# Optimization experiments

Measured on AMD Instinct MI355X. Metric: run time of the kernel, lower is better.

Reference implementation:

```python
import jax, jax.numpy as jnp
import numpy as np

N_SRC = 100000
N_DST = 100000
N_EDGES = 300000
FEAT = 256
REV_DIM = 128
REV_VOCAB = 500000


def setup_inputs() -> dict:
    key = jax.random.key(0)
    ks = jax.random.split(key, 14)
    feat = jax.random.normal(ks[0], (N_SRC, FEAT), dtype=jnp.float32)
    cj = jax.random.uniform(ks[1], (N_SRC, 1), dtype=jnp.float32)
    ci = jax.random.uniform(ks[2], (N_DST, 1), dtype=jnp.float32)
    edge_src = jax.random.randint(ks[3], (N_EDGES,), 0, N_SRC)
    edge_dst = jax.random.randint(ks[4], (N_EDGES,), 0, N_DST)
    review_id = jax.random.randint(ks[5], (N_EDGES,), 0, REV_VOCAB)
    s = 0.05
    review_emb = jax.random.normal(ks[6], (REV_VOCAB, REV_DIM), dtype=jnp.float32) * s
    prob_w = jax.random.normal(ks[7], (1, REV_DIM), dtype=jnp.float32) * s      # prob_score
    score_w = jax.random.normal(ks[8], (1, REV_DIM), dtype=jnp.float32) * s     # review_score
    rw1 = jax.random.normal(ks[9], (FEAT, REV_DIM), dtype=jnp.float32) * s      # review_w[0]
    rw2 = jax.random.normal(ks[10], (FEAT, FEAT), dtype=jnp.float32) * s        # review_w[2]
    rw3 = jax.random.normal(ks[11], (FEAT, FEAT), dtype=jnp.float32) * s        # review_w[4]
    lin_w = jax.random.normal(ks[12], (FEAT, FEAT), dtype=jnp.float32) * s      # self.linear
    lin_b = jax.random.normal(ks[13], (FEAT,), dtype=jnp.float32) * s
    return dict(feat=feat, cj=cj, ci=ci, edge_src=edge_src, edge_dst=edge_dst,
                review_id=review_id, review_emb=review_emb, prob_w=prob_w,
                score_w=score_w, rw1=rw1, rw2=rw2, rw3=rw3, lin_w=lin_w, lin_b=lin_b)


def reference(feat, cj, ci, edge_src, edge_dst, review_id,
              review_emb, prob_w, score_w, rw1, rw2, rw3, lin_w, lin_b):
    gelu = lambda x: jax.nn.gelu(x, approximate=False)  # torch default GELU (erf)
    # gather review embeddings per edge: [E, 128]
    rfeat = review_emb[review_id]
    pa = jax.nn.sigmoid(rfeat @ prob_w.T)    # [E, 1]
    ra = jax.nn.sigmoid(rfeat @ score_w.T)   # [E, 1]
    # review_w MLP: 128 -> F -> F -> F, no bias, GELU between
    rf = gelu(gelu(rfeat @ rw1.T) @ rw2.T) @ rw3.T  # [E, F]
    # per-edge message, gated and normalized by src cj (dropout is identity at p=0)
    m = (feat[edge_src] * pa + rf * ra) * cj[edge_src]  # [E, F]
    # scatter-sum to destination nodes
    h = jax.ops.segment_sum(m, edge_dst, num_segments=N_DST)  # [N_dst, F]
    rst = h * ci
    return rst @ lin_w.T + lin_b
```

## Files before the change

### kernel.cpp

```cpp
#include <hip/hip_runtime.h>
#include <math.h>
#include <stdint.h>


typedef short bf16x8 __attribute__((ext_vector_type(8)));
typedef float f32x16 __attribute__((ext_vector_type(16)));

__device__ __forceinline__ float bf2f(unsigned short v) {
    union { unsigned int u; float f; } x; x.u = ((unsigned int)v) << 16; return x.f;
}
__device__ __forceinline__ unsigned short f2bf(float f) {
    union { float f; unsigned int u; } x; x.f = f;
    unsigned int u = x.u;
    return (unsigned short)((u + 0x7FFFu + ((u >> 16) & 1u)) >> 16);
}
__device__ __forceinline__ unsigned pack2(float lo, float hi) {
    unsigned r;
    asm("v_cvt_pk_bf16_f32 %0, %1, %2" : "=v"(r) : "v"(lo), "v"(hi));
    return r;
}
__device__ __forceinline__ float gelu_fast(float x) {
    float e = __builtin_amdgcn_exp2f(x * -2.4554912f);
    return x * __builtin_amdgcn_rcpf(e + 1.0f);
}
__device__ __forceinline__ float sigmoidf(float x) {
    return 1.0f / (1.0f + expf(-x));
}

__global__ __launch_bounds__(256) void prep_weights(
    const float* __restrict__ rw1, const float* __restrict__ rw2,
    const float* __restrict__ rw3, const float* __restrict__ lw,
    unsigned short* __restrict__ w1s, unsigned short* __restrict__ w2s,
    unsigned short* __restrict__ w3s, unsigned short* __restrict__ lws)
{
    int i = blockIdx.x * blockDim.x + threadIdx.x;
    int j   = i & 7;
    int l   = (i >> 3) & 31;
    int kgg = (i >> 8) & 1;
    int n2  = (i >> 9) & 7;
    int ks  = i >> 12;
    if (i < 32768) {
        w1s[i] = f2bf(rw1[(n2 * 32 + l) * 128 + ks * 16 + kgg * 8 + j]);
    }
    if (i < 65536) {
        int row = n2 * 32 + l, k = ks * 16 + kgg * 8 + j;
        w2s[i] = f2bf(rw2[(size_t)row * 256 + k]);
        w3s[i] = f2bf(rw3[(size_t)row * 256 + k]);
        lws[i] = f2bf(lw[(size_t)row * 256 + k]);
    }
}

__device__ __forceinline__ bf16x8 ldw(const unsigned short* __restrict__ W,
                                      int ks, int nglob, int kg, int l31) {
    return *(const bf16x8*)(W + (((((ks * 8 + nglob) * 2) + kg) * 32 + l31) << 3));
}

__global__ __launch_bounds__(256) void hist_kernel(
    const int* __restrict__ edst, int* __restrict__ cnt,
    int* __restrict__ within, int E)
{
    int e = blockIdx.x * blockDim.x + threadIdx.x;
    if (e < E) within[e] = atomicAdd(&cnt[edst[e]], 1);
}

__global__ __launch_bounds__(1024) void scan_block(
    const int* __restrict__ cnt, int* __restrict__ start,
    int* __restrict__ bsum, int n)
{
    __shared__ int s[1024];
    int gid = blockIdx.x * 1024 + threadIdx.x;
    int v = (gid < n) ? cnt[gid] : 0;
    s[threadIdx.x] = v;
    __syncthreads();
    #pragma unroll
    for (int off = 1; off < 1024; off <<= 1) {
        int t = (threadIdx.x >= off) ? s[threadIdx.x - off] : 0;
        __syncthreads();
        if (threadIdx.x >= off) s[threadIdx.x] += t;
        __syncthreads();
    }
    if (gid < n) start[gid] = s[threadIdx.x] - v;
    if (threadIdx.x == 1023) bsum[blockIdx.x] = s[1023];
}

__global__ void scan_bsum(int* __restrict__ bsum, int nb) {
    if (threadIdx.x == 0 && blockIdx.x == 0) {
        int acc = 0;
        for (int i = 0; i < nb; ++i) { int v = bsum[i]; bsum[i] = acc; acc += v; }
    }
}

__global__ __launch_bounds__(1024) void add_offsets(
    int* __restrict__ start, const int* __restrict__ bsum, int n, int E)
{
    int gid = blockIdx.x * 1024 + threadIdx.x;
    if (gid < n) start[gid] += bsum[gid >> 10];
    if (gid == 0) start[n] = E;
}

__global__ __launch_bounds__(256) void build_sorted(
    const int* __restrict__ edst, const int* __restrict__ within,
    const int* __restrict__ start, const int* __restrict__ rid,
    const int* __restrict__ esrc, int* __restrict__ rid_s,
    int* __restrict__ esrc_s, int E)
{
    int e = blockIdx.x * blockDim.x + threadIdx.x;
    if (e < E) {
        int pos = start[edst[e]] + within[e];
        rid_s[pos]  = rid[e];
        esrc_s[pos] = esrc[e];
    }
}

__device__ __forceinline__ bf16x8 ldtf(const unsigned short* t_lds, int row, int ks, int kg) {
    int slot = (ks * 2 + kg) ^ (row & 15);
    return *(const bf16x8*)((const char*)t_lds + row * 512 + slot * 16);
}
__device__ __forceinline__ void sttf(unsigned short* t_lds, int row, int nn, int p, int kg, uint2 w) {
    int slot = (nn * 4 + p) ^ (row & 15);
    *(uint2*)((char*)t_lds + row * 512 + slot * 16 + kg * 8) = w;
}
__device__ __forceinline__ bf16x8 ldrb(const unsigned short* t_rb, int row, int ks, int kg) {
    int slot = (ks * 2 + kg) ^ (row & 15);
    return *(const bf16x8*)((const char*)t_rb + row * 256 + slot * 16);
}

__global__ __launch_bounds__(256, 3) void fused_edge(
    const float* __restrict__ remb, const int* __restrict__ rid_s,
    const int* __restrict__ esrc_s,
    const unsigned short* __restrict__ w1s, const unsigned short* __restrict__ w2s,
    const unsigned short* __restrict__ w3s,
    const float* __restrict__ pw, const float* __restrict__ sw,
    const float* __restrict__ cj, float* __restrict__ ga,
    unsigned short* __restrict__ m, int E)
{
    __shared__ __align__(16) unsigned short t_lds[64 * 256];
    __shared__ __align__(16) unsigned short t_rb[64 * 128];
    __shared__ float gvb_lds[64];

    const int lane = threadIdx.x & 63;
    const int f    = threadIdx.x >> 6;
    const int l31  = lane & 31;
    const int kg   = lane >> 5;
    const int blk0 = blockIdx.x * 64;

    {
        const int t = threadIdx.x;
        #pragma unroll
        for (int p = 0; p < 4; ++p) {
            int sIdx = p * 256 + t;
            int row  = sIdx >> 4;
            int c16  = sIdx & 15;
            int gr   = blk0 + row;
            int rr   = rid_s[(gr < E) ? gr : (E - 1)];
            const float* sp = remb + (size_t)rr * 128 + c16 * 8;
            float4 a = *(const float4*)sp;
            float4 b = *(const float4*)(sp + 4);
            uint4 w;
            w.x = pack2(a.x, a.y); w.y = pack2(a.z, a.w);
            w.z = pack2(b.x, b.y); w.w = pack2(b.z, b.w);
            int slot = c16 ^ (row & 15);
            *(uint4*)((char*)t_rb + row * 256 + slot * 16) = w;
        }
    }
    __syncthreads();

    {
        f32x16 acc[2][2];
        #pragma unroll
        for (int g = 0; g < 2; ++g) { acc[g][0] = (f32x16)0.0f; acc[g][1] = (f32x16)0.0f; }
        float pd0 = 0.f, rd0 = 0.f, pd1 = 0.f, rd1 = 0.f;

        #pragma unroll
        for (int ks = 0; ks < 8; ++ks) {
            bf16x8 wf0 = ldw(w1s, ks, f * 2 + 0, kg, l31);
            bf16x8 wf1 = ldw(w1s, ks, f * 2 + 1, kg, l31);
            #pragma unroll
            for (int g = 0; g < 2; ++g) {
                bf16x8 af = ldrb(t_rb, g * 32 + l31, ks, kg);
                if (f == 0) {
                    const int kk = ks * 16 + kg * 8;
                    float4 p0 = *(const float4*)(pw + kk), p1 = *(const float4*)(pw + kk + 4);
                    float4 s0 = *(const float4*)(sw + kk), s1v = *(const float4*)(sw + kk + 4);
                    float v0 = bf2f((unsigned short)af[0]), v1 = bf2f((unsigned short)af[1]);
                    float v2 = bf2f((unsigned short)af[2]), v3 = bf2f((unsigned short)af[3]);
                    float v4 = bf2f((unsigned short)af[4]), v5 = bf2f((unsigned short)af[5]);
                    float v6 = bf2f((unsigned short)af[6]), v7 = bf2f((unsigned short)af[7]);
                    float dp = v0*p0.x + v1*p0.y + v2*p0.z + v3*p0.w
                             + v4*p1.x + v5*p1.y + v6*p1.z + v7*p1.w;
                    float dr = v0*s0.x + v1*s0.y + v2*s0.z + v3*s0.w
                             + v4*s1v.x + v5*s1v.y + v6*s1v.z + v7*s1v.w;
                    if (g == 0) { pd0 += dp; rd0 += dr; } else { pd1 += dp; rd1 += dr; }
                }
                acc[g][0] = __builtin_amdgcn_mfma_f32_32x32x16_bf16(wf0, af, acc[g][0], 0, 0, 0);
                acc[g][1] = __builtin_amdgcn_mfma_f32_32x32x16_bf16(wf1, af, acc[g][1], 0, 0, 0);
            }
        }

        if (f == 0) {
            pd0 += __shfl_xor(pd0, 32); rd0 += __shfl_xor(rd0, 32);
            pd1 += __shfl_xor(pd1, 32); rd1 += __shfl_xor(rd1, 32);
            if (lane < 32) {
                int i0 = blk0 + l31, i1 = blk0 + 32 + l31;
                float cj0 = cj[esrc_s[(i0 < E) ? i0 : (E - 1)]];
                float cj1 = cj[esrc_s[(i1 < E) ? i1 : (E - 1)]];
                if (i0 < E) ga[i0] = sigmoidf(pd0) * cj0;
                if (i1 < E) ga[i1] = sigmoidf(pd1) * cj1;
                gvb_lds[l31]      = sigmoidf(rd0) * cj0;
                gvb_lds[32 + l31] = sigmoidf(rd1) * cj1;
            }
        }

        #pragma unroll
        for (int g = 0; g < 2; ++g)
            #pragma unroll
            for (int n = 0; n < 2; ++n)
                #pragma unroll
                for (int p = 0; p < 4; ++p) {
                    uint2 w;
                    w.x = pack2(gelu_fast(acc[g][n][4*p + 0]), gelu_fast(acc[g][n][4*p + 1]));
                    w.y = pack2(gelu_fast(acc[g][n][4*p + 2]), gelu_fast(acc[g][n][4*p + 3]));
                    sttf(t_lds, g * 32 + l31, f * 2 + n, p, kg, w);
                }
    }
    __syncthreads();

    {
        f32x16 acc[2][2];
        #pragma unroll
        for (int g = 0; g < 2; ++g) { acc[g][0] = (f32x16)0.0f; acc[g][1] = (f32x16)0.0f; }

        #pragma unroll
        for (int ks = 0; ks < 16; ++ks) {
            bf16x8 wf0 = ldw(w2s, ks, f * 2 + 0, kg, l31);
            bf16x8 wf1 = ldw(w2s, ks, f * 2 + 1, kg, l31);
            #pragma unroll
            for (int g = 0; g < 2; ++g) {
                bf16x8 tf = ldtf(t_lds, g * 32 + l31, ks, kg);
                acc[g][0] = __builtin_amdgcn_mfma_f32_32x32x16_bf16(wf0, tf, acc[g][0], 0, 0, 0);
                acc[g][1] = __builtin_amdgcn_mfma_f32_32x32x16_bf16(wf1, tf, acc[g][1], 0, 0, 0);
            }
        }
        __syncthreads();
        #pragma unroll
        for (int g = 0; g < 2; ++g)
            #pragma unroll
            for (int n = 0; n < 2; ++n)
                #pragma unroll
                for (int p = 0; p < 4; ++p) {
                    uint2 w;
                    w.x = pack2(gelu_fast(acc[g][n][4*p + 0]), gelu_fast(acc[g][n][4*p + 1]));
                    w.y = pack2(gelu_fast(acc[g][n][4*p + 2]), gelu_fast(acc[g][n][4*p + 3]));
                    sttf(t_lds, g * 32 + l31, f * 2 + n, p, kg, w);
                }
    }
    __syncthreads();

    {
        f32x16 acc[2][2];
        #pragma unroll
        for (int g = 0; g < 2; ++g) { acc[g][0] = (f32x16)0.0f; acc[g][1] = (f32x16)0.0f; }

        #pragma unroll
        for (int ks = 0; ks < 16; ++ks) {
            bf16x8 wf0 = ldw(w3s, ks, f * 2 + 0, kg, l31);
            bf16x8 wf1 = ldw(w3s, ks, f * 2 + 1, kg, l31);
            #pragma unroll
            for (int g = 0; g < 2; ++g) {
                bf16x8 tf = ldtf(t_lds, g * 32 + l31, ks, kg);
                acc[g][0] = __builtin_amdgcn_mfma_f32_32x32x16_bf16(tf, wf0, acc[g][0], 0, 0, 0);
                acc[g][1] = __builtin_amdgcn_mfma_f32_32x32x16_bf16(tf, wf1, acc[g][1], 0, 0, 0);
            }
        }

        #pragma unroll
        for (int g = 0; g < 2; ++g)
            #pragma unroll
            for (int r = 0; r < 16; ++r) {
                const int lrow = (r & 3) + 8 * (r >> 2) + 4 * kg;
                const int gi = blk0 + g * 32 + lrow;
                float gbv = gvb_lds[g * 32 + lrow];
                float v0 = acc[g][0][r] * gbv;
                float v1 = acc[g][1][r] * gbv;
                float o0 = __shfl_xor(v0, 1);
                float o1 = __shfl_xor(v1, 1);
                if (gi < E && (l31 & 1) == 0) {
                    unsigned short* mp = m + (size_t)gi * 256 + f * 64 + l31;
                    *(unsigned*)mp        = pack2(v0, o0);
                    *(unsigned*)(mp + 32) = pack2(v1, o1);
                }
            }
    }
}

__global__ __launch_bounds__(256) void segsum_kernel(
    const int* __restrict__ start, const unsigned short* __restrict__ m,
    const float* __restrict__ ga, const int* __restrict__ esrc_s,
    const float* __restrict__ feat, unsigned short* __restrict__ h, int ND)
{
    int d = blockIdx.x * 4 + (threadIdx.x >> 6);
    if (d >= ND) return;
    int lane = threadIdx.x & 63;
    int coff = lane * 4;
    int s0 = start[d], s1 = start[d + 1];
    float a0 = 0.f, a1 = 0.f, a2 = 0.f, a3 = 0.f;
    for (int base = s0; base < s1; base += 4) {
        float gav[4], msk[4];
        const float* fp[4];
        const unsigned short* mp[4];
        #pragma unroll
        for (int j = 0; j < 4; ++j) {
            int idx = base + j;
            bool v  = idx < s1;
            int ic  = v ? idx : (s1 - 1);
            msk[j]  = v ? 1.f : 0.f;
            gav[j]  = ga[ic] * msk[j];
            fp[j]   = feat + (size_t)esrc_s[ic] * 256 + coff;
            mp[j]   = m + (size_t)ic * 256 + coff;
        }
        #pragma unroll
        for (int j = 0; j < 4; ++j) {
            float4 fv = *(const float4*)fp[j];
            ushort4 v4 = *(const ushort4*)mp[j];
            a0 += bf2f(v4.x) * msk[j] + fv.x * gav[j];
            a1 += bf2f(v4.y) * msk[j] + fv.y * gav[j];
            a2 += bf2f(v4.z) * msk[j] + fv.z * gav[j];
            a3 += bf2f(v4.w) * msk[j] + fv.w * gav[j];
        }
    }
    ushort4 o; o.x = f2bf(a0); o.y = f2bf(a1); o.z = f2bf(a2); o.w = f2bf(a3);
    *(ushort4*)(h + (size_t)d * 256 + coff) = o;
}

__global__ __launch_bounds__(256, 2) void g4_kernel(
    const unsigned short* __restrict__ Ab, const unsigned short* __restrict__ lws,
    float* __restrict__ outf, const float* __restrict__ ci,
    const float* __restrict__ bias, int M)
{
    const int lane = threadIdx.x & 63;
    const int wid  = threadIdx.x >> 6;
    const int l31  = lane & 31;
    const int kg   = lane >> 5;
    const int f    = wid & 1;
    const int wbase = blockIdx.x * 128 + (wid >> 1) * 64;
    const int r0 = wbase + l31, r1 = wbase + 32 + l31;
    const int ar0 = (r0 < M) ? r0 : (M - 1);
    const int ar1 = (r1 < M) ? r1 : (M - 1);

    f32x16 acc[2][4];
    #pragma unroll
    for (int mi = 0; mi < 2; ++mi)
        #pragma unroll
        for (int n = 0; n < 4; ++n) acc[mi][n] = (f32x16)0.0f;

    #pragma unroll
    for (int ks = 0; ks < 16; ++ks) {
        const int kk = ks * 16 + kg * 8;
        bf16x8 a0 = *(const bf16x8*)(Ab + (size_t)ar0 * 256 + kk);
        bf16x8 a1 = *(const bf16x8*)(Ab + (size_t)ar1 * 256 + kk);
        #pragma unroll
        for (int n = 0; n < 4; ++n) {
            bf16x8 b = ldw(lws, ks, f * 4 + n, kg, l31);
            acc[0][n] = __builtin_amdgcn_mfma_f32_32x32x16_bf16(a0, b, acc[0][n], 0, 0, 0);
            acc[1][n] = __builtin_amdgcn_mfma_f32_32x32x16_bf16(a1, b, acc[1][n], 0, 0, 0);
        }
    }
    #pragma unroll
    for (int mi = 0; mi < 2; ++mi) {
        #pragma unroll
        for (int r = 0; r < 16; ++r) {
            const int gr = wbase + mi * 32 + (r & 3) + 8 * (r >> 2) + 4 * kg;
            if (gr >= M) continue;
            float civ = ci[gr];
            #pragma unroll
            for (int n = 0; n < 4; ++n) {
                int col = f * 128 + n * 32 + l31;
                outf[(size_t)gr * 256 + col] = acc[mi][n][r] * civ + bias[col];
            }
        }
    }
}

extern "C" void kernel_launch(void* const* d_in, const int* in_sizes, int n_in,
                              void* d_out, int out_size, void* d_ws, size_t ws_size,
                              hipStream_t stream) {
    const float* feat = (const float*)d_in[0];
    const float* cj   = (const float*)d_in[1];
    const float* ci   = (const float*)d_in[2];
    const int*   esrc = (const int*)d_in[3];
    const int*   edst = (const int*)d_in[4];
    const int*   rid  = (const int*)d_in[5];
    const float* remb = (const float*)d_in[6];
    const float* pw   = (const float*)d_in[7];
    const float* sw   = (const float*)d_in[8];
    const float* rw1  = (const float*)d_in[9];
    const float* rw2  = (const float*)d_in[10];
    const float* rw3  = (const float*)d_in[11];
    const float* lw   = (const float*)d_in[12];
    const float* lb   = (const float*)d_in[13];
    float* out = (float*)d_out;

    const int E  = in_sizes[3];
    const int ND = in_sizes[2];

    char* ws = (char*)d_ws;
    float* ga = (float*)ws;
    unsigned short* m   = (unsigned short*)(ga + E);
    unsigned short* h   = m + (size_t)E * 256;
    unsigned short* w1s = h + (size_t)ND * 256;
    unsigned short* w2s = w1s + 32768;
    unsigned short* w3s = w2s + 65536;
    unsigned short* lws = w3s + 65536;
    int* cnt    = (int*)(lws + 65536);
    int* start  = cnt + ND;
    int* bsum   = start + ND + 1;
    int* within = bsum + 128;
    int* rid_s  = within + E;
    int* esrc_s = rid_s + E;

    const int NB = (ND + 1023) / 1024;

    hipMemsetAsync(cnt, 0, (size_t)ND * sizeof(int), stream);
    prep_weights<<<256, 256, 0, stream>>>(rw1, rw2, rw3, lw, w1s, w2s, w3s, lws);

    hist_kernel<<<(E + 255) / 256, 256, 0, stream>>>(edst, cnt, within, E);
    scan_block<<<NB, 1024, 0, stream>>>(cnt, start, bsum, ND);
    scan_bsum<<<1, 64, 0, stream>>>(bsum, NB);
    add_offsets<<<NB, 1024, 0, stream>>>(start, bsum, ND, E);
    build_sorted<<<(E + 255) / 256, 256, 0, stream>>>(edst, within, start, rid, esrc,
                                                      rid_s, esrc_s, E);

    fused_edge<<<(E + 63) / 64, 256, 0, stream>>>(
        remb, rid_s, esrc_s, w1s, w2s, w3s, pw, sw, cj, ga, m, E);

    segsum_kernel<<<(ND + 3) / 4, 256, 0, stream>>>(start, m, ga, esrc_s, feat, h, ND);

    g4_kernel<<<(ND + 127) / 128, 256, 0, stream>>>(h, lws, out, ci, lb, ND);
}
```

Before: 358.9 us.

## Split fused_edge output columns across eight waves instead of four

Doubles the fused edge-MLP block to 512 threads, so each of the 8 waves owns one 32-column output slice instead of two. Per-wave accumulator state halves, from four 32x32 tiles to two, which should lower VGPR pressure and allow more resident waves to hide gather and MFMA latency. The cost is that each B-operand fragment loaded from LDS now feeds one MFMA instead of two, so LDS read traffic per MFMA rises, and the larger blocks make barriers more expensive.

```diff
diff --git a/kernel.cpp b/kernel.cpp
--- a/kernel.cpp
+++ b/kernel.cpp
@@ -125,7 +125,7 @@
     return *(const bf16x8*)((const char*)t_rb + row * 256 + slot * 16);
 }
 
-__global__ __launch_bounds__(256, 3) void fused_edge(
+__global__ __launch_bounds__(512, 4) void fused_edge(
     const float* __restrict__ remb, const int* __restrict__ rid_s,
     const int* __restrict__ esrc_s,
     const unsigned short* __restrict__ w1s, const unsigned short* __restrict__ w2s,
@@ -147,8 +147,8 @@
     {
         const int t = threadIdx.x;
         #pragma unroll
-        for (int p = 0; p < 4; ++p) {
-            int sIdx = p * 256 + t;
+        for (int p = 0; p < 2; ++p) {
+            int sIdx = p * 512 + t;
             int row  = sIdx >> 4;
             int c16  = sIdx & 15;
             int gr   = blk0 + row;
@@ -166,15 +166,13 @@
     __syncthreads();
 
     {
-        f32x16 acc[2][2];
-        #pragma unroll
-        for (int g = 0; g < 2; ++g) { acc[g][0] = (f32x16)0.0f; acc[g][1] = (f32x16)0.0f; }
+        f32x16 acc[2];
+        acc[0] = (f32x16)0.0f; acc[1] = (f32x16)0.0f;
         float pd0 = 0.f, rd0 = 0.f, pd1 = 0.f, rd1 = 0.f;
 
         #pragma unroll
         for (int ks = 0; ks < 8; ++ks) {
-            bf16x8 wf0 = ldw(w1s, ks, f * 2 + 0, kg, l31);
-            bf16x8 wf1 = ldw(w1s, ks, f * 2 + 1, kg, l31);
+            bf16x8 wf = ldw(w1s, ks, f, kg, l31);
             #pragma unroll
             for (int g = 0; g < 2; ++g) {
                 bf16x8 af = ldrb(t_rb, g * 32 + l31, ks, kg);
@@ -192,8 +190,7 @@
                              + v4*s1v.x + v5*s1v.y + v6*s1v.z + v7*s1v.w;
                     if (g == 0) { pd0 += dp; rd0 += dr; } else { pd1 += dp; rd1 += dr; }
                 }
-                acc[g][0] = __builtin_amdgcn_mfma_f32_32x32x16_bf16(wf0, af, acc[g][0], 0, 0, 0);
-                acc[g][1] = __builtin_amdgcn_mfma_f32_32x32x16_bf16(wf1, af, acc[g][1], 0, 0, 0);
+                acc[g] = __builtin_amdgcn_mfma_f32_32x32x16_bf16(wf, af, acc[g], 0, 0, 0);
             }
         }
 
@@ -214,62 +211,52 @@
         #pragma unroll
         for (int g = 0; g < 2; ++g)
             #pragma unroll
-            for (int n = 0; n < 2; ++n)
-                #pragma unroll
-                for (int p = 0; p < 4; ++p) {
-                    uint2 w;
-                    w.x = pack2(gelu_fast(acc[g][n][4*p + 0]), gelu_fast(acc[g][n][4*p + 1]));
-                    w.y = pack2(gelu_fast(acc[g][n][4*p + 2]), gelu_fast(acc[g][n][4*p + 3]));
-                    sttf(t_lds, g * 32 + l31, f * 2 + n, p, kg, w);
-                }
+            for (int p = 0; p < 4; ++p) {
+                uint2 w;
+                w.x = pack2(gelu_fast(acc[g][4*p + 0]), gelu_fast(acc[g][4*p + 1]));
+                w.y = pack2(gelu_fast(acc[g][4*p + 2]), gelu_fast(acc[g][4*p + 3]));
+                sttf(t_lds, g * 32 + l31, f, p, kg, w);
+            }
     }
     __syncthreads();
 
     {
-        f32x16 acc[2][2];
-        #pragma unroll
-        for (int g = 0; g < 2; ++g) { acc[g][0] = (f32x16)0.0f; acc[g][1] = (f32x16)0.0f; }
+        f32x16 acc[2];
+        acc[0] = (f32x16)0.0f; acc[1] = (f32x16)0.0f;
 
         #pragma unroll
         for (int ks = 0; ks < 16; ++ks) {
-            bf16x8 wf0 = ldw(w2s, ks, f * 2 + 0, kg, l31);
-            bf16x8 wf1 = ldw(w2s, ks, f * 2 + 1, kg, l31);
+            bf16x8 wf = ldw(w2s, ks, f, kg, l31);
             #pragma unroll
             for (int g = 0; g < 2; ++g) {
                 bf16x8 tf = ldtf(t_lds, g * 32 + l31, ks, kg);
-                acc[g][0] = __builtin_amdgcn_mfma_f32_32x32x16_bf16(wf0, tf, acc[g][0], 0, 0, 0);
-                acc[g][1] = __builtin_amdgcn_mfma_f32_32x32x16_bf16(wf1, tf, acc[g][1], 0, 0, 0);
+                acc[g] = __builtin_amdgcn_mfma_f32_32x32x16_bf16(wf, tf, acc[g], 0, 0, 0);
             }
         }
         __syncthreads();
         #pragma unroll
         for (int g = 0; g < 2; ++g)
             #pragma unroll
-            for (int n = 0; n < 2; ++n)
-                #pragma unroll
-                for (int p = 0; p < 4; ++p) {
-                    uint2 w;
-                    w.x = pack2(gelu_fast(acc[g][n][4*p + 0]), gelu_fast(acc[g][n][4*p + 1]));
-                    w.y = pack2(gelu_fast(acc[g][n][4*p + 2]), gelu_fast(acc[g][n][4*p + 3]));
-                    sttf(t_lds, g * 32 + l31, f * 2 + n, p, kg, w);
-                }
+            for (int p = 0; p < 4; ++p) {
+                uint2 w;
+                w.x = pack2(gelu_fast(acc[g][4*p + 0]), gelu_fast(acc[g][4*p + 1]));
+                w.y = pack2(gelu_fast(acc[g][4*p + 2]), gelu_fast(acc[g][4*p + 3]));
+                sttf(t_lds, g * 32 + l31, f, p, kg, w);
+            }
     }
     __syncthreads();
 
     {
-        f32x16 acc[2][2];
-        #pragma unroll
-        for (int g = 0; g < 2; ++g) { acc[g][0] = (f32x16)0.0f; acc[g][1] = (f32x16)0.0f; }
+        f32x16 acc[2];
+        acc[0] = (f32x16)0.0f; acc[1] = (f32x16)0.0f;
 
         #pragma unroll
         for (int ks = 0; ks < 16; ++ks) {
-            bf16x8 wf0 = ldw(w3s, ks, f * 2 + 0, kg, l31);
-            bf16x8 wf1 = ldw(w3s, ks, f * 2 + 1, kg, l31);
+            bf16x8 wf = ldw(w3s, ks, f, kg, l31);
             #pragma unroll
             for (int g = 0; g < 2; ++g) {
                 bf16x8 tf = ldtf(t_lds, g * 32 + l31, ks, kg);
-                acc[g][0] = __builtin_amdgcn_mfma_f32_32x32x16_bf16(tf, wf0, acc[g][0], 0, 0, 0);
-                acc[g][1] = __builtin_amdgcn_mfma_f32_32x32x16_bf16(tf, wf1, acc[g][1], 0, 0, 0);
+                acc[g] = __builtin_amdgcn_mfma_f32_32x32x16_bf16(tf, wf, acc[g], 0, 0, 0);
             }
         }
 
@@ -280,14 +267,10 @@
                 const int lrow = (r & 3) + 8 * (r >> 2) + 4 * kg;
                 const int gi = blk0 + g * 32 + lrow;
                 float gbv = gvb_lds[g * 32 + lrow];
-                float v0 = acc[g][0][r] * gbv;
-                float v1 = acc[g][1][r] * gbv;
+                float v0 = acc[g][r] * gbv;
                 float o0 = __shfl_xor(v0, 1);
-                float o1 = __shfl_xor(v1, 1);
                 if (gi < E && (l31 & 1) == 0) {
-                    unsigned short* mp = m + (size_t)gi * 256 + f * 64 + l31;
-                    *(unsigned*)mp        = pack2(v0, o0);
-                    *(unsigned*)(mp + 32) = pack2(v1, o1);
+                    *(unsigned*)(m + (size_t)gi * 256 + f * 32 + l31) = pack2(v0, o0);
                 }
             }
     }
@@ -430,7 +413,7 @@
     build_sorted<<<(E + 255) / 256, 256, 0, stream>>>(edst, within, start, rid, esrc,
                                                       rid_s, esrc_s, E);
 
-    fused_edge<<<(E + 63) / 64, 256, 0, stream>>>(
+    fused_edge<<<(E + 63) / 64, 512, 0, stream>>>(
         remb, rid_s, esrc_s, w1s, w2s, w3s, pw, sw, cj, ga, m, E);
 
     segsum_kernel<<<(ND + 3) / 4, 256, 0, stream>>>(start, m, ga, esrc_s, feat, h, ND);
```

Measured after the change: 390.8 us. 8.9% more time.
